# Kernel optimization log

Measured on AMD Instinct MI355X. Metric: run time of the kernel, lower is better.

## Reference

```python
import jax, jax.numpy as jnp
import numpy as np

V = 5000      # output_class_dim
E = 512       # embed_dim
F = 512       # 2 * listener_hidden_dim
H = 512       # speller_hidden_dim
HEADS = 4
HD = F // HEADS  # 128
STEPS = 64    # max_label_len
B, T = 32, 1024


def setup_inputs() -> dict:
    key = jax.random.key(0)
    ks = jax.random.split(key, 10)
    s = 0.05
    return {
        "listener_feature": jax.random.normal(ks[0], (B, T, F), jnp.float32),
        "embedding": jax.random.normal(ks[1], (V, E), jnp.float32) * s,
        # LSTM cell (single layer, torch gate order i,f,g,o)
        "W_ih": jax.random.normal(ks[2], (4 * H, E + F), jnp.float32) * s,
        "W_hh": jax.random.normal(ks[3], (4 * H, H), jnp.float32) * s,
        "b_ih": jax.random.normal(ks[4], (4 * H,), jnp.float32) * s,
        "b_hh": jax.random.normal(ks[5], (4 * H,), jnp.float32) * s,
        # predict_hid: Linear(2H -> 512)
        "Wp": jax.random.normal(ks[6], (512, 2 * H), jnp.float32) * s,
        "bp": jax.random.normal(ks[7], (512,), jnp.float32) * s,
        # character_distribution: Linear(512 -> V)
        "Wc": jax.random.normal(ks[8], (V, 512), jnp.float32) * s,
        "bc": jax.random.normal(ks[9], (V,), jnp.float32) * s,
    }


def _decode(listener_feature, embedding, W_ih, W_hh, b_ih, b_hh, Wp, bp, Wc, bc):
    b = listener_feature.shape[0]
    lf_heads = listener_feature.reshape(b, T, HEADS, HD)  # [B,T,h,d]

    def lstm_cell(x, h, c):
        gates = x @ W_ih.T + h @ W_hh.T + (b_ih + b_hh)
        i, f, g, o = jnp.split(gates, 4, axis=-1)
        c_new = jax.nn.sigmoid(f) * c + jax.nn.sigmoid(i) * jnp.tanh(g)
        h_new = jax.nn.sigmoid(o) * jnp.tanh(c_new)
        return h_new, c_new

    def step(carry, _):
        h, c, rnn_in = carry
        h, c = lstm_cell(rnn_in, h, c)                       # rnn_output = h [B,H]
        ds = h.reshape(b, HEADS, HD)                          # decoder state per head
        energy = jnp.einsum('bhd,bthd->bht', ds, lf_heads)    # dot attention
        scores = jax.nn.softmax(energy, axis=-1)              # [B,h,T]
        context = jnp.einsum('bht,bthd->bhd', scores, lf_heads).reshape(b, F)
        concat = jnp.concatenate([h, context], axis=-1)       # [B,2H]
        hid = jnp.maximum(concat @ Wp.T + bp, 0.0)            # ReLU MLP
        raw_pred = jax.nn.log_softmax(hid @ Wc.T + bc, axis=-1)
        # greedy feedback (teacher_force_rate = 0 since ground_truth is None)
        tok = jnp.argmax(raw_pred, axis=-1)                   # [B]
        rnn_in_next = jnp.concatenate([embedding[tok], context], axis=-1)
        return (h, c, rnn_in_next), (raw_pred, scores[:, -1, :])

    h0 = jnp.zeros((b, H), listener_feature.dtype)
    c0 = jnp.zeros((b, H), listener_feature.dtype)
    # initial input: embedding of token 0, concat first listener frame
    emb0 = jnp.broadcast_to(embedding[0], (b, E))
    rnn_in0 = jnp.concatenate([emb0, listener_feature[:, 0, :]], axis=-1)

    _, (raw_pred_seq, attn_seq) = jax.lax.scan(step, (h0, c0, rnn_in0), None, length=STEPS)
    return raw_pred_seq, attn_seq  # [S,B,V], [S,B,T] (last head, as in original)


def reference(listener_feature, embedding, W_ih, W_hh, b_ih, b_hh, Wp, bp, Wc, bc):
    return _decode(listener_feature, embedding, W_ih, W_hh, b_ih, b_hh, Wp, bp, Wc, bc)
```

## Files before the change

kernel.cpp:

```cpp
#include <hip/hip_runtime.h>
#include <math.h>
#include <stdint.h>


#define NB 512
#define NT 256

constexpr int Tv = 1024, Vv = 5000, STEPS = 64;

constexpr int MCNT = 0;
constexpr int GEN  = 16;
constexpr int GCNT = 64;
constexpr int GFLG = 1024;
constexpr int ACNT = 2048;
constexpr int LCNT = 2560;
constexpr int WSU  = 4096;

constexpr int XH   = 0;
constexpr int HB   = XH + 32*1024;
constexpr int HID  = HB + 2*32*512;
constexpr int PART = HID + 32*512;
constexpr int E3   = PART + 32*4*16*130;
constexpr int PM   = E3 + 32*1024;
constexpr int PSUM = PM + 32*256;
constexpr int PIDX = PSUM + 32*256;
constexpr int MLS  = PIDX + 32*256;

__device__ __forceinline__ float sigm(float x) { return 1.f / (1.f + expf(-x)); }

__device__ __forceinline__ float ld4(const float* p) {
  return __hip_atomic_load(const_cast<float*>(p), __ATOMIC_RELAXED, __HIP_MEMORY_SCOPE_AGENT);
}
__device__ __forceinline__ void st4(float* p, float v) {
  __hip_atomic_store(p, v, __ATOMIC_RELAXED, __HIP_MEMORY_SCOPE_AGENT);
}
__device__ __forceinline__ float2 ld8(const float* p) {
  unsigned long long u = __hip_atomic_load(
      reinterpret_cast<unsigned long long*>(const_cast<float*>(p)),
      __ATOMIC_RELAXED, __HIP_MEMORY_SCOPE_AGENT);
  union { unsigned long long u; float2 f; } c; c.u = u; return c.f;
}
__device__ __forceinline__ void st8(float* p, float2 v) {
  union { float2 f; unsigned long long u; } c; c.f = v;
  __hip_atomic_store(reinterpret_cast<unsigned long long*>(p), c.u,
                     __ATOMIC_RELAXED, __HIP_MEMORY_SCOPE_AGENT);
}
__device__ __forceinline__ int ld4i(const int* p) {
  return (int)__hip_atomic_load(reinterpret_cast<unsigned*>(const_cast<int*>(p)),
                                __ATOMIC_RELAXED, __HIP_MEMORY_SCOPE_AGENT);
}
__device__ __forceinline__ void st4i(int* p, int v) {
  __hip_atomic_store(reinterpret_cast<unsigned*>(p), (unsigned)v,
                     __ATOMIC_RELAXED, __HIP_MEMORY_SCOPE_AGENT);
}
__device__ __forceinline__ unsigned ld_rlx(unsigned* p) {
  return __hip_atomic_load(p, __ATOMIC_RELAXED, __HIP_MEMORY_SCOPE_AGENT);
}
__device__ __forceinline__ void st_rlx(unsigned* p, unsigned v) {
  __hip_atomic_store(p, v, __ATOMIC_RELAXED, __HIP_MEMORY_SCOPE_AGENT);
}
__device__ __forceinline__ unsigned add_rlx(unsigned* p, unsigned v) {
  return __hip_atomic_fetch_add(p, v, __ATOMIC_RELAXED, __HIP_MEMORY_SCOPE_AGENT);
}

__device__ __forceinline__ void gsync(unsigned* wsu, int blk, int tid, unsigned& myGen) {
  __syncthreads();
  if (tid == 0) {
    const unsigned target = ++myGen;
    const int grp = blk >> 4;
    unsigned o = add_rlx(&wsu[GCNT + grp*16], 1u);
    if (o == target*16u - 1u) {
      unsigned o2 = add_rlx(&wsu[MCNT], 1u);
      if (o2 == target*32u - 1u) st_rlx(&wsu[GEN], target);
    }
    if ((blk & 15) == 0) {
      while (ld_rlx(&wsu[GEN]) != target) __builtin_amdgcn_s_sleep(2);
      st_rlx(&wsu[GFLG + grp*32], target);
    } else {
      while (ld_rlx(&wsu[GFLG + grp*32]) != target) __builtin_amdgcn_s_sleep(2);
    }
  }
  __syncthreads();
}

__global__ void speller_init(const float* __restrict__ LF, const float* __restrict__ Emb,
                             float* __restrict__ wsf, unsigned* __restrict__ wsu) {
  int b = blockIdx.x;
  for (int i = threadIdx.x; i < 512; i += NT) {
    st4(wsf + XH + b*1024 + i,       Emb[i]);
    st4(wsf + XH + b*1024 + 512 + i, LF[(size_t)b*Tv*512 + i]);
    st4(wsf + HB + b*512 + i,        0.f);
  }
  if (b == 0) for (int i = threadIdx.x; i < WSU; i += NT) st_rlx(wsu + i, 0u);
}

struct LdsA { float Wg[8][1536]; float gb[8]; };
struct LdsB { float Wc[20][512]; float Wp[2][1024]; float bcl[20]; float bpl[2]; };
union  LdsU { LdsA a; LdsB b; };

__launch_bounds__(NT, 2)
__global__ void speller_main(const float* __restrict__ LF, const float* __restrict__ Emb,
                             const float* __restrict__ Wih, const float* __restrict__ Whh,
                             const float* __restrict__ bih, const float* __restrict__ bhh,
                             const float* __restrict__ Wp,  const float* __restrict__ bp,
                             const float* __restrict__ Wc,  const float* __restrict__ bc,
                             float* __restrict__ out, unsigned* __restrict__ wsu,
                             float* __restrict__ wsf) {
  const int blk = blockIdx.x, tid = threadIdx.x;
  unsigned myGen = 0;
  __shared__ LdsU lds;
  __shared__ float scr[784];
  __shared__ int  sint[300];

  const int ab = blk >> 4, atc = blk & 15;
  const int aw = tid >> 6, aln = tid & 63;

  float4 lfr[32];
  {
    const float4* src = (const float4*)(LF +
        (((size_t)ab*Tv + atc*64 + aln)*512 + aw*128));
#pragma unroll
    for (int q = 0; q < 32; ++q) lfr[q] = src[q];
  }

  if (blk < 256) {
    const int u0 = blk * 2;
    for (int idx = tid; idx < 8*1536; idx += NT) {
      int r = idx / 1536, k = idx - r*1536;
      int g = r >> 1, uu = r & 1;
      int row = g*512 + u0 + uu;
      lds.a.Wg[r][k] = (k < 1024) ? Wih[(size_t)row*1024 + k]
                                  : Whh[(size_t)row*512 + (k-1024)];
    }
    if (tid < 8) {
      int g = tid >> 1, uu = tid & 1, row = g*512 + u0 + uu;
      lds.a.gb[tid] = bih[row] + bhh[row];
    }
  } else {
    const int blk2 = blk - 256, v0 = blk2*20, rp0 = blk2*2;
    if (v0 < Vv) {
      for (int idx = tid; idx < 20*512; idx += NT) {
        int vi = idx >> 9, k = idx & 511;
        lds.b.Wc[vi][k] = Wc[(size_t)(v0+vi)*512 + k];
      }
      if (tid < 20) lds.b.bcl[tid] = bc[v0+tid];
    }
    for (int idx = tid; idx < 2048; idx += NT) {
      int r = idx >> 10, k = idx & 1023;
      lds.b.Wp[r][k] = Wp[(size_t)(rp0+r)*1024 + k];
    }
    if (tid < 2) lds.b.bpl[tid] = bp[rp0+tid];
  }
  __syncthreads();

  float c_reg[2][4];
#pragma unroll
  for (int uu = 0; uu < 2; ++uu)
#pragma unroll
    for (int i = 0; i < 4; ++i) c_reg[uu][i] = 0.f;
  float lgv[20];

#pragma unroll 1
  for (int s = 0; s < STEPS; ++s) {
    const int rbuf = s & 1, wbuf = (s + 1) & 1;

    if (blk < 256) {
      const int u0 = blk * 2;
      const int slot = tid >> 5, ks = tid & 31, b0 = slot * 4;
      float acc[8][4];
#pragma unroll
      for (int r = 0; r < 8; ++r)
#pragma unroll
        for (int i = 0; i < 4; ++i) acc[r][i] = 0.f;
      const float* x1 = wsf + XH;
      const float* x2 = wsf + HB + rbuf*16384;
#pragma unroll 2
      for (int q = 0; q < 8; ++q) {
        const int kq = q*32 + ks;
        float2 xa[4], xb[4];
#pragma unroll
        for (int i = 0; i < 4; ++i) {
          const float* p = x1 + (size_t)(b0+i)*1024 + kq*4;
          xa[i] = ld8(p); xb[i] = ld8(p + 2);
        }
#pragma unroll
        for (int r = 0; r < 8; ++r) {
          float4 wv = *(const float4*)(&lds.a.Wg[r][kq*4]);
#pragma unroll
          for (int i = 0; i < 4; ++i)
            acc[r][i] += wv.x*xa[i].x + wv.y*xa[i].y + wv.z*xb[i].x + wv.w*xb[i].y;
        }
      }
#pragma unroll 2
      for (int q = 0; q < 4; ++q) {
        const int kq = q*32 + ks;
        float2 xa[4], xb[4];
#pragma unroll
        for (int i = 0; i < 4; ++i) {
          const float* p = x2 + (size_t)(b0+i)*512 + kq*4;
          xa[i] = ld8(p); xb[i] = ld8(p + 2);
        }
#pragma unroll
        for (int r = 0; r < 8; ++r) {
          float4 wv = *(const float4*)(&lds.a.Wg[r][1024 + kq*4]);
#pragma unroll
          for (int i = 0; i < 4; ++i)
            acc[r][i] += wv.x*xa[i].x + wv.y*xa[i].y + wv.z*xb[i].x + wv.w*xb[i].y;
        }
      }
#pragma unroll
      for (int r = 0; r < 8; ++r)
#pragma unroll
        for (int i = 0; i < 4; ++i) {
          float v = acc[r][i];
          v += __shfl_xor(v, 16); v += __shfl_xor(v, 8); v += __shfl_xor(v, 4);
          v += __shfl_xor(v, 2);  v += __shfl_xor(v, 1);
          acc[r][i] = v + lds.a.gb[r];
        }
      float hnew[2][4];
#pragma unroll
      for (int uu = 0; uu < 2; ++uu)
#pragma unroll
        for (int i = 0; i < 4; ++i) {
          float cn = sigm(acc[2+uu][i]) * c_reg[uu][i]
                   + sigm(acc[uu][i]) * tanhf(acc[4+uu][i]);
          c_reg[uu][i] = cn;
          hnew[uu][i] = sigm(acc[6+uu][i]) * tanhf(cn);
        }
      if (ks == 0) {
#pragma unroll
        for (int i = 0; i < 4; ++i)
          st8(wsf + HB + wbuf*16384 + (size_t)(b0+i)*512 + u0,
              make_float2(hnew[0][i], hnew[1][i]));
      }
    } else if (s > 0) {
      const int blk2 = blk - 256;
      if (blk2 < 250) {
        const int v0 = blk2 * 20, bb = tid >> 3, ks = tid & 7;
        if (ks == 0) {
          float2 ml = ld8(wsf + MLS + 2*bb);
          float sub = ml.x + ml.y;
#pragma unroll
          for (int vi = 0; vi < 20; ++vi)
            out[(size_t)(s-1)*160000 + (size_t)bb*5000 + v0 + vi] = lgv[vi] - sub;
        }
      }
    }
    gsync(wsu, blk, tid, myGen);

    {
      float* hs = scr;
      {
        float2 hv = ld8(wsf + HB + wbuf*16384 + (size_t)ab*512 + tid*2);
        hs[tid*2] = hv.x; hs[tid*2+1] = hv.y;
      }
      __syncthreads();
      float e = 0.f;
      {
        const float4* hp = (const float4*)(hs + aw*128);
#pragma unroll
        for (int q = 0; q < 32; ++q) {
          float4 f = lfr[q], hh = hp[q];
          e += f.x*hh.x + f.y*hh.y + f.z*hh.z + f.w*hh.w;
        }
      }
      float m = e;
#pragma unroll
      for (int off = 32; off; off >>= 1) m = fmaxf(m, __shfl_xor(m, off));
      float p = expf(e - m);
      float l = p;
#pragma unroll
      for (int off = 32; off; off >>= 1) l += __shfl_xor(l, off);
      if (aw == 3) st4(wsf + E3 + (size_t)ab*1024 + atc*64 + aln, e);
      float* pr = wsf + PART + (size_t)((ab*4 + aw)*16 + atc)*130;
#pragma unroll
      for (int ch = 0; ch < 2; ++ch) {
        float c[64];
#pragma unroll
        for (int q = 0; q < 16; ++q) {
          float4 f = lfr[ch*16 + q];
          c[4*q+0] = p*f.x; c[4*q+1] = p*f.y; c[4*q+2] = p*f.z; c[4*q+3] = p*f.w;
        }
#pragma unroll
        for (int o = 32; o >= 1; o >>= 1) {
#pragma unroll
          for (int j = 0; j < 32; ++j) {
            if (j < o) {
              float keep = (aln & o) ? c[j + o] : c[j];
              float send = (aln & o) ? c[j] : c[j + o];
              c[j] = keep + __shfl_xor(send, o);
            }
          }
        }
        st4(pr + 2 + ch*64 + aln, c[0]);
      }
      if (aln == 0) st8(pr, make_float2(m, l));
      __syncthreads();
      if (tid == 0) {
        unsigned old = add_rlx(&wsu[ACNT + ab*16], 1u);
        sint[0] = (old == (unsigned)(s*16 + 15));
      }
      __syncthreads();
      if (sint[0]) {
        const int w2 = tid >> 6, ln2 = tid & 63;
        const float* pb = wsf + PART + (size_t)(ab*4 + w2)*16*130;
        float M = -1e30f;
        float mv[16], lv[16];
#pragma unroll
        for (int i = 0; i < 16; ++i) { float2 t = ld8(pb + i*130); mv[i] = t.x; lv[i] = t.y; M = fmaxf(M, t.x); }
        float L = 0.f;
        float sc[16];
#pragma unroll
        for (int i = 0; i < 16; ++i) { sc[i] = expf(mv[i] - M); L += lv[i] * sc[i]; }
        float cc0 = 0.f, cc1 = 0.f;
#pragma unroll
        for (int i = 0; i < 16; ++i) {
          float2 cx = ld8(pb + i*130 + 2 + 2*ln2);
          cc0 += sc[i]*cx.x; cc1 += sc[i]*cx.y;
        }
        float invL = 1.f / L;
        st8(wsf + XH + (size_t)ab*1024 + 512 + w2*128 + 2*ln2,
            make_float2(cc0*invL, cc1*invL));
        if (ln2 == 0) { scr[768 + w2*2] = M; scr[769 + w2*2] = L; }
        __syncthreads();
        float M3 = scr[768 + 6], iL3 = 1.f / scr[768 + 7];
        for (int i = tid; i < 1024; i += NT)
          out[(size_t)10240000 + ((size_t)(s*32 + ab))*1024 + i] =
              expf(ld4(wsf + E3 + (size_t)ab*1024 + i) - M3) * iL3;
      }
    }
    gsync(wsu, blk, tid, myGen);

    if (blk >= 256) {
      const int blk2 = blk - 256, rp0 = blk2*2;
      const int bb = tid & 31, ks = tid >> 5;
      const float* xr = (ks < 4) ? (wsf + HB + wbuf*16384 + (size_t)bb*512 + ks*128)
                                 : (wsf + XH + (size_t)bb*1024 + (ks-4)*128 + 512);
      const int kb = ks * 128;
      const float4* w0 = (const float4*)(&lds.b.Wp[0][kb]);
      const float4* w1 = (const float4*)(&lds.b.Wp[1][kb]);
      float a0 = 0.f, a1 = 0.f;
#pragma unroll 8
      for (int q = 0; q < 32; ++q) {
        float2 xva = ld8(xr + q*4), xvb = ld8(xr + q*4 + 2);
        float4 wv0 = w0[q], wv1 = w1[q];
        a0 += wv0.x*xva.x + wv0.y*xva.y + wv0.z*xvb.x + wv0.w*xvb.y;
        a1 += wv1.x*xva.x + wv1.y*xva.y + wv1.z*xvb.x + wv1.w*xvb.y;
      }
      scr[ks*32 + bb] = a0; scr[256 + ks*32 + bb] = a1;
      __syncthreads();
      if (tid < 64) {
        int r = tid >> 5, b2 = tid & 31;
        float ssum = 0.f;
#pragma unroll
        for (int j = 0; j < 8; ++j) ssum += scr[r*256 + j*32 + b2];
        ssum += lds.b.bpl[r];
        st4(wsf + HID + (size_t)b2*512 + rp0 + r, fmaxf(ssum, 0.f));
      }
      __syncthreads();
    }
    gsync(wsu, blk, tid, myGen);

    if (blk >= 256) {
      const int blk2 = blk - 256;
      if (blk2 < 250) {
        const int v0 = blk2 * 20;
        const int bb = tid >> 3, ks = tid & 7;
#pragma unroll
        for (int vi = 0; vi < 20; ++vi) lgv[vi] = 0.f;
        const float* hb = wsf + HID + (size_t)bb*512;
#pragma unroll 1
        for (int half = 0; half < 2; ++half) {
          float4 xr[8];
#pragma unroll
          for (int q = 0; q < 8; ++q) {
            const float* p = hb + ((half*8 + q)*8 + ks)*4;
            float2 a = ld8(p), b2v = ld8(p + 2);
            xr[q] = make_float4(a.x, a.y, b2v.x, b2v.y);
          }
#pragma unroll
          for (int vi = 0; vi < 20; ++vi) {
            float a = 0.f;
#pragma unroll
            for (int q = 0; q < 8; ++q) {
              float4 wv = *(const float4*)(&lds.b.Wc[vi][((half*8 + q)*8 + ks)*4]);
              a += wv.x*xr[q].x + wv.y*xr[q].y + wv.z*xr[q].z + wv.w*xr[q].w;
            }
            lgv[vi] += a;
          }
        }
#pragma unroll
        for (int vi = 0; vi < 20; ++vi) {
          float a = lgv[vi];
          a += __shfl_xor(a, 1); a += __shfl_xor(a, 2); a += __shfl_xor(a, 4);
          lgv[vi] = a + lds.b.bcl[vi];
        }
        float mych = lgv[0]; int ami = 0;
#pragma unroll
        for (int vi = 1; vi < 20; ++vi)
          if (lgv[vi] > mych) { mych = lgv[vi]; ami = vi; }
        float sume = 0.f;
#pragma unroll
        for (int vi = 0; vi < 20; ++vi) sume += expf(lgv[vi] - mych);
        if (ks == 0) {
          st4(wsf + PM + bb*256 + blk2, mych);
          st4(wsf + PSUM + bb*256 + blk2, sume);
          st4i((int*)(wsf + PIDX) + bb*256 + blk2, v0 + ami);
        }
      }
      __syncthreads();
      if (tid == 0 && blk2 < 250) add_rlx(&wsu[LCNT], 1u);
      if (blk2 < 32) {
        const int b2 = blk2;
        if (tid == 0) {
          while (ld_rlx(&wsu[LCNT]) < (unsigned)((s + 1) * 250))
            __builtin_amdgcn_s_sleep(2);
        }
        __syncthreads();
        float mv = -1e30f, sv = 0.f; int iv = 0x7fffffff;
        if (tid < 250) {
          mv = ld4(wsf + PM + b2*256 + tid);
          sv = ld4(wsf + PSUM + b2*256 + tid);
          iv = ld4i((const int*)(wsf + PIDX) + b2*256 + tid);
        }
        scr[tid] = mv; sint[40 + tid] = iv;
        __syncthreads();
        for (int off = 128; off; off >>= 1) {
          if (tid < off) {
            float m2 = scr[tid + off]; int i2 = sint[40 + tid + off];
            if (m2 > scr[tid] || (m2 == scr[tid] && i2 < sint[40 + tid])) {
              scr[tid] = m2; sint[40 + tid] = i2;
            }
          }
          __syncthreads();
        }
        float M = scr[0]; int tok = sint[40];
        __syncthreads();
        scr[tid] = sv * expf(mv - M);
        __syncthreads();
        for (int off = 128; off; off >>= 1) {
          if (tid < off) scr[tid] += scr[tid + off];
          __syncthreads();
        }
        if (tid == 0) st8(wsf + MLS + 2*b2, make_float2(M, logf(scr[0])));
        for (int i = tid; i < 256; i += NT) {
          const float2* er = (const float2*)(Emb + (size_t)tok*512);
          st8(wsf + XH + (size_t)b2*1024 + 2*i, er[i]);
        }
      }
    }
    gsync(wsu, blk, tid, myGen);
  }

  if (blk >= 256) {
    const int blk2 = blk - 256;
    if (blk2 < 250) {
      const int v0 = blk2 * 20, bb = tid >> 3, ks = tid & 7;
      if (ks == 0) {
        float2 ml = ld8(wsf + MLS + 2*bb);
        float sub = ml.x + ml.y;
#pragma unroll
        for (int vi = 0; vi < 20; ++vi)
          out[(size_t)63*160000 + (size_t)bb*5000 + v0 + vi] = lgv[vi] - sub;
      }
    }
  }
}

extern "C" void kernel_launch(void* const* d_in, const int* in_sizes, int n_in,
                              void* d_out, int out_size, void* d_ws, size_t ws_size,
                              hipStream_t stream) {
  (void)in_sizes; (void)n_in; (void)out_size; (void)ws_size;
  const float* LF  = (const float*)d_in[0];
  const float* Emb = (const float*)d_in[1];
  const float* Wih = (const float*)d_in[2];
  const float* Whh = (const float*)d_in[3];
  const float* bih = (const float*)d_in[4];
  const float* bhh = (const float*)d_in[5];
  const float* Wp  = (const float*)d_in[6];
  const float* bp  = (const float*)d_in[7];
  const float* Wc  = (const float*)d_in[8];
  const float* bc  = (const float*)d_in[9];
  float* out = (float*)d_out;
  unsigned* wsu = (unsigned*)d_ws;
  float* wsf = (float*)d_ws + WSU;

  speller_init<<<32, NT, 0, stream>>>(LF, Emb, wsf, wsu);
  speller_main<<<NB, NT, 0, stream>>>(LF, Emb, Wih, Whh, bih, bhh, Wp, bp, Wc, bc,
                                      out, wsu, wsf);
}
```

Baseline: 6.742 ms.

## Precompute context and hidden-state gate partials during idle phase of LSTM blocks

The LSTM gate matvec is split so that the context-half and recurrent-h part of the gate accumulation are computed early, in a later phase of the previous step when the LSTM blocks would otherwise idle while other blocks run the projection. Only the embedding part stays on the critical path after the token is chosen. Thread mapping also changes from 32-way to 16-way k-split with 2 batches per slot, shortening the shuffle reduction. Correctness depends on the context and h buffers being final when that earlier phase runs.

```diff
diff --git a/kernel.cpp b/kernel.cpp
--- a/kernel.cpp
+++ b/kernel.cpp
@@ -97,6 +97,45 @@
 struct LdsA { float Wg[8][1536]; float gb[8]; };
 struct LdsB { float Wc[20][512]; float Wp[2][1024]; float bcl[20]; float bpl[2]; };
 union  LdsU { LdsA a; LdsB b; };
+
+__device__ __forceinline__ void gate_accum_A(float acc[8][2], const float* __restrict__ wsf,
+                                             const float (&Wg)[8][1536],
+                                             int ks, int b0, int hbuf) {
+#pragma unroll 2
+  for (int q = 0; q < 8; ++q) {
+    const int k4 = 512 + (q*16 + ks)*4;
+    float2 xa[2], xb[2];
+#pragma unroll
+    for (int i = 0; i < 2; ++i) {
+      const float* p = wsf + XH + (size_t)(b0+i)*1024 + k4;
+      xa[i] = ld8(p); xb[i] = ld8(p + 2);
+    }
+#pragma unroll
+    for (int r = 0; r < 8; ++r) {
+      float4 wv = *(const float4*)(&Wg[r][k4]);
+#pragma unroll
+      for (int i = 0; i < 2; ++i)
+        acc[r][i] += wv.x*xa[i].x + wv.y*xa[i].y + wv.z*xb[i].x + wv.w*xb[i].y;
+    }
+  }
+#pragma unroll 2
+  for (int q = 0; q < 8; ++q) {
+    const int k4 = (q*16 + ks)*4;
+    float2 xa[2], xb[2];
+#pragma unroll
+    for (int i = 0; i < 2; ++i) {
+      const float* p = wsf + HB + hbuf*16384 + (size_t)(b0+i)*512 + k4;
+      xa[i] = ld8(p); xb[i] = ld8(p + 2);
+    }
+#pragma unroll
+    for (int r = 0; r < 8; ++r) {
+      float4 wv = *(const float4*)(&Wg[r][1024 + k4]);
+#pragma unroll
+      for (int i = 0; i < 2; ++i)
+        acc[r][i] += wv.x*xa[i].x + wv.y*xa[i].y + wv.z*xb[i].x + wv.w*xb[i].y;
+    }
+  }
+}
 
 __launch_bounds__(NT, 2)
 __global__ void speller_main(const float* __restrict__ LF, const float* __restrict__ Emb,
@@ -153,75 +192,61 @@
   }
   __syncthreads();
 
-  float c_reg[2][4];
+  float acc[8][2];
+  float c_reg[2][2];
 #pragma unroll
   for (int uu = 0; uu < 2; ++uu)
 #pragma unroll
-    for (int i = 0; i < 4; ++i) c_reg[uu][i] = 0.f;
+    for (int i = 0; i < 2; ++i) c_reg[uu][i] = 0.f;
   float lgv[20];
+
+  if (blk < 256) {
+    const int ks = tid & 15, b0 = (tid >> 4) * 2;
+#pragma unroll
+    for (int r = 0; r < 8; ++r)
+#pragma unroll
+      for (int i = 0; i < 2; ++i) acc[r][i] = 0.f;
+    gate_accum_A(acc, wsf, lds.a.Wg, ks, b0, 0);
+  }
 
 #pragma unroll 1
   for (int s = 0; s < STEPS; ++s) {
-    const int rbuf = s & 1, wbuf = (s + 1) & 1;
+    const int wbuf = (s + 1) & 1;
 
     if (blk < 256) {
       const int u0 = blk * 2;
-      const int slot = tid >> 5, ks = tid & 31, b0 = slot * 4;
-      float acc[8][4];
-#pragma unroll
-      for (int r = 0; r < 8; ++r)
-#pragma unroll
-        for (int i = 0; i < 4; ++i) acc[r][i] = 0.f;
-      const float* x1 = wsf + XH;
-      const float* x2 = wsf + HB + rbuf*16384;
+      const int ks = tid & 15, b0 = (tid >> 4) * 2;
 #pragma unroll 2
       for (int q = 0; q < 8; ++q) {
-        const int kq = q*32 + ks;
-        float2 xa[4], xb[4];
-#pragma unroll
-        for (int i = 0; i < 4; ++i) {
-          const float* p = x1 + (size_t)(b0+i)*1024 + kq*4;
+        const int k4 = (q*16 + ks)*4;
+        float2 xa[2], xb[2];
+#pragma unroll
+        for (int i = 0; i < 2; ++i) {
+          const float* p = wsf + XH + (size_t)(b0+i)*1024 + k4;
           xa[i] = ld8(p); xb[i] = ld8(p + 2);
         }
 #pragma unroll
         for (int r = 0; r < 8; ++r) {
-          float4 wv = *(const float4*)(&lds.a.Wg[r][kq*4]);
-#pragma unroll
-          for (int i = 0; i < 4; ++i)
+          float4 wv = *(const float4*)(&lds.a.Wg[r][k4]);
+#pragma unroll
+          for (int i = 0; i < 2; ++i)
             acc[r][i] += wv.x*xa[i].x + wv.y*xa[i].y + wv.z*xb[i].x + wv.w*xb[i].y;
         }
       }
-#pragma unroll 2
-      for (int q = 0; q < 4; ++q) {
-        const int kq = q*32 + ks;
-        float2 xa[4], xb[4];
-#pragma unroll
-        for (int i = 0; i < 4; ++i) {
-          const float* p = x2 + (size_t)(b0+i)*512 + kq*4;
-          xa[i] = ld8(p); xb[i] = ld8(p + 2);
-        }
-#pragma unroll
-        for (int r = 0; r < 8; ++r) {
-          float4 wv = *(const float4*)(&lds.a.Wg[r][1024 + kq*4]);
-#pragma unroll
-          for (int i = 0; i < 4; ++i)
-            acc[r][i] += wv.x*xa[i].x + wv.y*xa[i].y + wv.z*xb[i].x + wv.w*xb[i].y;
-        }
-      }
 #pragma unroll
       for (int r = 0; r < 8; ++r)
 #pragma unroll
-        for (int i = 0; i < 4; ++i) {
+        for (int i = 0; i < 2; ++i) {
           float v = acc[r][i];
-          v += __shfl_xor(v, 16); v += __shfl_xor(v, 8); v += __shfl_xor(v, 4);
-          v += __shfl_xor(v, 2);  v += __shfl_xor(v, 1);
+          v += __shfl_xor(v, 8); v += __shfl_xor(v, 4);
+          v += __shfl_xor(v, 2); v += __shfl_xor(v, 1);
           acc[r][i] = v + lds.a.gb[r];
         }
-      float hnew[2][4];
+      float hnew[2][2];
 #pragma unroll
       for (int uu = 0; uu < 2; ++uu)
 #pragma unroll
-        for (int i = 0; i < 4; ++i) {
+        for (int i = 0; i < 2; ++i) {
           float cn = sigm(acc[2+uu][i]) * c_reg[uu][i]
                    + sigm(acc[uu][i]) * tanhf(acc[4+uu][i]);
           c_reg[uu][i] = cn;
@@ -229,7 +254,7 @@
         }
       if (ks == 0) {
 #pragma unroll
-        for (int i = 0; i < 4; ++i)
+        for (int i = 0; i < 2; ++i)
           st8(wsf + HB + wbuf*16384 + (size_t)(b0+i)*512 + u0,
               make_float2(hnew[0][i], hnew[1][i]));
       }
@@ -358,6 +383,13 @@
         st4(wsf + HID + (size_t)b2*512 + rp0 + r, fmaxf(ssum, 0.f));
       }
       __syncthreads();
+    } else if (s < 63) {
+      const int ks = tid & 15, b0 = (tid >> 4) * 2;
+#pragma unroll
+      for (int r = 0; r < 8; ++r)
+#pragma unroll
+        for (int i = 0; i < 2; ++i) acc[r][i] = 0.f;
+      gate_accum_A(acc, wsf, lds.a.Wg, ks, b0, wbuf);
     }
     gsync(wsu, blk, tid, myGen);
 
```

New measurement: 6.665 ms. No clear change (-1.1%).
